# Optimization experiments

Hardware: AMD Instinct MI355X
Metric: run time of the kernel (lower is better)

Reference implementation:

```python
import jax, jax.numpy as jnp
import numpy as np
from bisect import bisect

# hyperparameters (from init_kwargs)
DELTA = 1e-4
GAMMA = 0.1
UTILITY_SCALE = -0.01
PRIORITY_RAIL = 0.5
LOSS_BALANCE = 1.0
ALPHA_ELU = 1.0
ENTROPY_THRESHOLDS = [0, 10, 50]
ENTROPY_LEVELS = [0.0, 0.05, 0.1, 1.0]
MASK_LEVEL = 10000.0

N = 512


def setup_inputs() -> dict:
    key = jax.random.key(0)
    k1, k2, k3, k4 = jax.random.split(key, 4)
    soft_adj = jax.random.uniform(k1, (N, N), dtype=jnp.float32)
    # original adjacency is a binary {0,1} float mask
    original_adj = (jax.random.uniform(k2, (N, N)) > 0.5).astype(jnp.float32)
    distances = jax.random.uniform(k3, (N, N), dtype=jnp.float32) * 100.0
    flow = jax.random.uniform(k4, (N, N), dtype=jnp.float32) * 10.0
    epoch = 20  # python int, selects entropy penalty level via bisect
    return {"soft_adj": soft_adj, "original_adj": original_adj,
            "distances": distances, "flow": flow, "epoch": epoch}


def _shortest_path(soft_adj, distances):
    """Soft (softmin via logsumexp) Floyd-Warshall all-pairs shortest path."""
    W = distances / (soft_adj + DELTA)          # [N, N] effective edge weights
    n = W.shape[0]
    w0 = W * (1.0 - jnp.eye(n, dtype=W.dtype))  # zero diagonal

    def step(w, k):
        # softmin(w, w[:,k,None] + w[None,k,:]) without materializing a stack
        path_through_k = w[:, k][:, None] + w[k, :][None, :]
        w_new = -GAMMA * jnp.logaddexp(-w / GAMMA, -path_through_k / GAMMA)
        return w_new, None

    w_dist, _ = jax.lax.scan(step, w0, jnp.arange(n))
    return w_dist


def reference(soft_adj, original_adj, distances, flow, epoch):
    loss_cost = jnp.sum(soft_adj * distances)

    shortest_paths = _shortest_path(soft_adj, distances)

    exp_ut_rail = jnp.exp(UTILITY_SCALE * shortest_paths * PRIORITY_RAIL)
    exp_ut_base = jnp.exp(UTILITY_SCALE * distances)
    choice_matrix = exp_ut_rail / (exp_ut_rail + exp_ut_base)
    distance_saved = distances - PRIORITY_RAIL * shortest_paths
    utility_gain = flow * choice_matrix * distance_saved
    utility_gain = jax.nn.elu(utility_gain, alpha=ALPHA_ELU) + ALPHA_ELU

    inverse_soft = jnp.eye(soft_adj.shape[0], dtype=soft_adj.dtype) - soft_adj
    entropy_loss = jnp.sum(jnp.square(soft_adj * inverse_soft))
    entropy_scale = ENTROPY_LEVELS[bisect(ENTROPY_THRESHOLDS, epoch)]

    mask_loss = jnp.sum(soft_adj * (1.0 - original_adj))

    return (loss_cost
            + LOSS_BALANCE * jnp.sum(utility_gain)
            + entropy_loss * entropy_scale
            + MASK_LEVEL * mask_loss)
```

## Files before the change

kernel.cpp:

```cpp
#include <hip/hip_runtime.h>
#include <math.h>

#define NN 512
#define KP 64
#define NPANEL 8
#define NTHR 256
#define NBLK 256
#define TRUNITS (448 * 112)

#define D_   0
#define V_   4160
#define B2_  8320
#define UB_  12672
#define SB_  17024
#define H_   21376
#define LDSN 25728

__device__ __forceinline__ float einit(const float* s, const float* dI, int i, int j) {
  float w = dI[i * NN + j] / (s[i * NN + j] + 1e-4f);
  if (i == j) w = 0.f;
  return expf(-10.f * w);
}

__global__ __launch_bounds__(NTHR) void fw_p0(
    const float* __restrict__ s, const float* __restrict__ dI,
    float* __restrict__ Cs, float* __restrict__ Rs, float* __restrict__ out) {
  __shared__ __align__(16) float lds[LDSN];
  const int blk = blockIdx.x, tid = threadIdx.x;
  const bool isC = (blk < 16);
  const int sb = (blk >> 1) & 7;
  const int h = blk & 1;
  const int sOff = sb * KP;
  const bool haveSl = (sb != 0);
  if (blk == 0 && tid == 0) out[0] = 0.f;

  for (int e = tid; e < 4096; e += NTHR) {
    const int a = e >> 6, b = e & 63;
    lds[D_ + a * 65 + b] = einit(s, dI, a, b);
  }
  if (haveSl) {
    if (isC) {
      for (int e = tid; e < 2048; e += NTHR) {
        const int a = 32 * h + (e >> 6), b = e & 63;
        lds[V_ + a * 65 + b] = einit(s, dI, sOff + a, b);
      }
    } else {
      for (int e = tid; e < 2048; e += NTHR) {
        const int m = e >> 5, j = 32 * h + (e & 31);
        lds[V_ + j * 65 + m] = einit(s, dI, m, sOff + j);
      }
    }
  }
  __syncthreads();

  if (tid < 64) {
    float x[64];
    if (isC) {
#pragma unroll
      for (int a = 0; a < 64; ++a) x[a] = lds[D_ + a * 65 + tid];
    } else {
#pragma unroll
      for (int a = 0; a < 64; ++a) x[a] = lds[D_ + tid * 65 + a];
    }
#pragma unroll
    for (int m = 0; m < 64; ++m) {
      const float xm = x[m];
      lds[H_ + m * 68 + tid] = xm;
#pragma unroll
      for (int a = 0; a < 64; ++a) {
        const int sa = __builtin_amdgcn_readlane(__float_as_int(x[a]), m);
        x[a] += __int_as_float(sa) * xm;
      }
    }
  } else if (tid < 192) {
    if (!haveSl) {
      for (int e = tid - 64; e < 4096; e += 128) {
        const int a = e >> 6, b = e & 63;
        lds[V_ + a * 65 + b] = isC ? lds[D_ + a * 65 + b] : lds[D_ + b * 65 + a];
      }
    }
  }
  __syncthreads();

  for (int cch = 0; cch < 4; ++cch) {
    const int mb = cch * 16;
    if (cch > 0 && tid < 128) {
      const int r = 32 * h + (tid & 31);
      const int g = tid >> 5;
      const int m0c = mb + 4 * g;
      const int vb = V_ + r * 65;
      float a0 = lds[vb + m0c + 0], a1 = lds[vb + m0c + 1];
      float a2 = lds[vb + m0c + 2], a3 = lds[vb + m0c + 3];
      for (int mp = 0; mp < mb; ++mp) {
        const float vr = lds[vb + mp];
        const float4 u4 = *(const float4*)&lds[H_ + mp * 68 + m0c];
        a0 += vr * u4.x; a1 += vr * u4.y; a2 += vr * u4.z; a3 += vr * u4.w;
      }
      lds[vb + m0c + 0] = a0; lds[vb + m0c + 1] = a1;
      lds[vb + m0c + 2] = a2; lds[vb + m0c + 3] = a3;
    }
    __syncthreads();
    if (tid < 32) {
      const int r = 32 * h + tid;
      const int vb = V_ + r * 65 + mb;
      float v[16];
#pragma unroll
      for (int u2 = 0; u2 < 16; ++u2) v[u2] = lds[vb + u2];
#pragma unroll
      for (int mp = 0; mp < 15; ++mp) {
        const float vmp = v[mp];
#pragma unroll
        for (int m2 = mp + 1; m2 < 16; ++m2)
          v[m2] += vmp * lds[H_ + (mb + mp) * 68 + (mb + m2)];
      }
#pragma unroll
      for (int u2 = 0; u2 < 16; ++u2) lds[vb + u2] = v[u2];
    }
    __syncthreads();
  }

  if (isC) {
    for (int e = tid; e < 2048; e += NTHR) {
      const int a = 32 * h + (e >> 6), b = e & 63;
      Cs[(size_t)(sOff + a) * KP + b] = lds[V_ + a * 65 + b];
    }
  } else {
    for (int e = tid; e < 2048; e += NTHR) {
      const int m = e >> 5, j = 32 * h + (e & 31);
      Rs[(size_t)m * NN + (sOff + j)] = lds[V_ + j * 65 + m];
    }
  }
}

__global__ __launch_bounds__(NTHR) void fw_phase(
    const float* __restrict__ s, const float* __restrict__ dI,
    float* __restrict__ E, float* __restrict__ Cs, float* __restrict__ Rs,
    int p) {
  __shared__ __align__(16) float lds[LDSN];
  const int blk = blockIdx.x, tid = threadIdx.x;
  const int k0 = p * KP;
  const float* Cprev = Cs + (size_t)(p - 1) * (NN * KP);
  const float* Rprev = Rs + (size_t)(p - 1) * (KP * NN);

  if (blk >= 32) {
    const int gt = (blk - 32) * NTHR + tid;
    if (gt >= TRUNITS) return;
    const int ii = gt / 112;
    const int jj = gt - ii * 112;
    const int i = (ii < k0) ? ii : ii + KP;
    const int j = ((jj < (p << 4)) ? jj : jj + 16) << 2;
    const int idx = i * NN + j;
    float4 acc;
    if (p == 1) {
      acc.x = einit(s, dI, i, j + 0);
      acc.y = einit(s, dI, i, j + 1);
      acc.z = einit(s, dI, i, j + 2);
      acc.w = einit(s, dI, i, j + 3);
    } else {
      acc = *(const float4*)(E + idx);
    }
    const float* crow = Cprev + (size_t)i * KP;
    const float* rcol = Rprev + j;
#pragma unroll 8
    for (int r = 0; r < KP; ++r) {
      const float cv = crow[r];
      const float4 rv = *(const float4*)(rcol + (size_t)r * NN);
      acc.x += cv * rv.x; acc.y += cv * rv.y;
      acc.z += cv * rv.z; acc.w += cv * rv.w;
    }
    *(float4*)(E + idx) = acc;
    return;
  }

  const bool isC = (blk < 16);
  const int sb = (blk >> 1) & 7;
  const int h = blk & 1;
  const int sOff = sb * KP;
  const bool haveSl = (sb != p);

  const int r0d = (tid >> 4) << 2, m0d = (tid & 15) << 2;
  float4 epre[4];
  if (p == 1) {
#pragma unroll
    for (int i2 = 0; i2 < 4; ++i2) {
      epre[i2].x = einit(s, dI, k0 + r0d + i2, k0 + m0d + 0);
      epre[i2].y = einit(s, dI, k0 + r0d + i2, k0 + m0d + 1);
      epre[i2].z = einit(s, dI, k0 + r0d + i2, k0 + m0d + 2);
      epre[i2].w = einit(s, dI, k0 + r0d + i2, k0 + m0d + 3);
    }
  } else {
#pragma unroll
    for (int i2 = 0; i2 < 4; ++i2)
      epre[i2] = *(const float4*)(E + (size_t)(k0 + r0d + i2) * NN + (k0 + m0d));
  }

#pragma unroll
  for (int k = 0; k < 4; ++k) {
    const int e4 = tid + k * NTHR;
    const int a = e4 >> 4, b4 = (e4 & 15) << 2;
    *(float4*)&lds[B2_ + a * 68 + b4] =
        *(const float4*)(Cprev + (size_t)(k0 + a) * KP + b4);
    *(float4*)&lds[UB_ + a * 68 + b4] =
        *(const float4*)(Rprev + (size_t)a * NN + (k0 + b4));
    if (haveSl) {
      if (isC)
        *(float4*)&lds[SB_ + a * 68 + b4] =
            *(const float4*)(Cprev + (size_t)(sOff + a) * KP + b4);
      else
        *(float4*)&lds[SB_ + a * 68 + b4] =
            *(const float4*)(Rprev + (size_t)a * NN + (sOff + b4));
    }
  }
  __syncthreads();

  {
    float acc[4][4];
#pragma unroll
    for (int i2 = 0; i2 < 4; ++i2) {
      acc[i2][0] = epre[i2].x; acc[i2][1] = epre[i2].y;
      acc[i2][2] = epre[i2].z; acc[i2][3] = epre[i2].w;
    }
    for (int rr = 0; rr < KP; ++rr) {
      const float4 b4 = *(const float4*)&lds[UB_ + rr * 68 + m0d];
#pragma unroll
      for (int i2 = 0; i2 < 4; ++i2) {
        const float av = lds[B2_ + (r0d + i2) * 68 + rr];
        acc[i2][0] += av * b4.x; acc[i2][1] += av * b4.y;
        acc[i2][2] += av * b4.z; acc[i2][3] += av * b4.w;
      }
    }
#pragma unroll
    for (int i2 = 0; i2 < 4; ++i2)
#pragma unroll
      for (int j2 = 0; j2 < 4; ++j2)
        lds[D_ + (r0d + i2) * 65 + (m0d + j2)] = acc[i2][j2];
  }
  __syncthreads();

  if (tid < 64) {
    float x[64];
    if (isC) {
#pragma unroll
      for (int a = 0; a < 64; ++a) x[a] = lds[D_ + a * 65 + tid];
    } else {
#pragma unroll
      for (int a = 0; a < 64; ++a) x[a] = lds[D_ + tid * 65 + a];
    }
#pragma unroll
    for (int m = 0; m < 64; ++m) {
      const float xm = x[m];
      lds[H_ + m * 68 + tid] = xm;
#pragma unroll
      for (int a = 0; a < 64; ++a) {
        const int sa = __builtin_amdgcn_readlane(__float_as_int(x[a]), m);
        x[a] += __int_as_float(sa) * xm;
      }
    }
  } else if (tid < 192) {
    const int tt = tid - 64;
    if (haveSl) {
      float acc[4][4];
      if (isC) {
        const int r0 = 32 * h + ((tt >> 4) << 2);
        const int m0 = (tt & 15) << 2;
        if (p == 1) {
#pragma unroll
          for (int i2 = 0; i2 < 4; ++i2) {
            acc[i2][0] = einit(s, dI, sOff + r0 + i2, k0 + m0 + 0);
            acc[i2][1] = einit(s, dI, sOff + r0 + i2, k0 + m0 + 1);
            acc[i2][2] = einit(s, dI, sOff + r0 + i2, k0 + m0 + 2);
            acc[i2][3] = einit(s, dI, sOff + r0 + i2, k0 + m0 + 3);
          }
        } else {
#pragma unroll
          for (int i2 = 0; i2 < 4; ++i2) {
            const float4 ev = *(const float4*)(E + (size_t)(sOff + r0 + i2) * NN + (k0 + m0));
            acc[i2][0] = ev.x; acc[i2][1] = ev.y; acc[i2][2] = ev.z; acc[i2][3] = ev.w;
          }
        }
        for (int rr = 0; rr < KP; ++rr) {
          const float4 b4 = *(const float4*)&lds[UB_ + rr * 68 + m0];
#pragma unroll
          for (int i2 = 0; i2 < 4; ++i2) {
            const float av = lds[SB_ + (r0 + i2) * 68 + rr];
            acc[i2][0] += av * b4.x; acc[i2][1] += av * b4.y;
            acc[i2][2] += av * b4.z; acc[i2][3] += av * b4.w;
          }
        }
#pragma unroll
        for (int i2 = 0; i2 < 4; ++i2) {
          *(float4*)(E + (size_t)(sOff + r0 + i2) * NN + (k0 + m0)) =
              make_float4(acc[i2][0], acc[i2][1], acc[i2][2], acc[i2][3]);
#pragma unroll
          for (int j2 = 0; j2 < 4; ++j2)
            lds[V_ + (r0 + i2) * 65 + (m0 + j2)] = acc[i2][j2];
        }
      } else {
        const int r0 = (tt & 15) << 2;
        const int c0 = 32 * h + ((tt >> 4) << 2);
        if (p == 1) {
#pragma unroll
          for (int i2 = 0; i2 < 4; ++i2) {
            acc[i2][0] = einit(s, dI, k0 + r0 + i2, sOff + c0 + 0);
            acc[i2][1] = einit(s, dI, k0 + r0 + i2, sOff + c0 + 1);
            acc[i2][2] = einit(s, dI, k0 + r0 + i2, sOff + c0 + 2);
            acc[i2][3] = einit(s, dI, k0 + r0 + i2, sOff + c0 + 3);
          }
        } else {
#pragma unroll
          for (int i2 = 0; i2 < 4; ++i2) {
            const float4 ev = *(const float4*)(E + (size_t)(k0 + r0 + i2) * NN + (sOff + c0));
            acc[i2][0] = ev.x; acc[i2][1] = ev.y; acc[i2][2] = ev.z; acc[i2][3] = ev.w;
          }
        }
        for (int rr = 0; rr < KP; ++rr) {
          const float4 b4 = *(const float4*)&lds[SB_ + rr * 68 + c0];
#pragma unroll
          for (int i2 = 0; i2 < 4; ++i2) {
            const float av = lds[B2_ + (r0 + i2) * 68 + rr];
            acc[i2][0] += av * b4.x; acc[i2][1] += av * b4.y;
            acc[i2][2] += av * b4.z; acc[i2][3] += av * b4.w;
          }
        }
#pragma unroll
        for (int i2 = 0; i2 < 4; ++i2) {
          *(float4*)(E + (size_t)(k0 + r0 + i2) * NN + (sOff + c0)) =
              make_float4(acc[i2][0], acc[i2][1], acc[i2][2], acc[i2][3]);
#pragma unroll
          for (int j2 = 0; j2 < 4; ++j2)
            lds[V_ + (c0 + j2) * 65 + (r0 + i2)] = acc[i2][j2];
        }
      }
    } else {
      for (int e = tt; e < 4096; e += 128) {
        const int a = e >> 6, b = e & 63;
        lds[V_ + a * 65 + b] = isC ? lds[D_ + a * 65 + b] : lds[D_ + b * 65 + a];
      }
    }
  } else {
    if (p == 1 && !haveSl && isC) {
      for (int e = 2048 * h + (tid - 192); e < 2048 * (h + 1); e += 64) {
        const int a = e >> 6, b = e & 63;
        E[(size_t)(k0 + a) * NN + (k0 + b)] = einit(s, dI, k0 + a, k0 + b);
      }
    }
  }
  __syncthreads();

  for (int cch = 0; cch < 4; ++cch) {
    const int mb = cch * 16;
    if (cch > 0 && tid < 128) {
      const int r = 32 * h + (tid & 31);
      const int g = tid >> 5;
      const int m0c = mb + 4 * g;
      const int vb = V_ + r * 65;
      float a0 = lds[vb + m0c + 0], a1 = lds[vb + m0c + 1];
      float a2 = lds[vb + m0c + 2], a3 = lds[vb + m0c + 3];
      for (int mp = 0; mp < mb; ++mp) {
        const float vr = lds[vb + mp];
        const float4 u4 = *(const float4*)&lds[H_ + mp * 68 + m0c];
        a0 += vr * u4.x; a1 += vr * u4.y; a2 += vr * u4.z; a3 += vr * u4.w;
      }
      lds[vb + m0c + 0] = a0; lds[vb + m0c + 1] = a1;
      lds[vb + m0c + 2] = a2; lds[vb + m0c + 3] = a3;
    }
    __syncthreads();
    if (tid < 32) {
      const int r = 32 * h + tid;
      const int vb = V_ + r * 65 + mb;
      float v[16];
#pragma unroll
      for (int u2 = 0; u2 < 16; ++u2) v[u2] = lds[vb + u2];
#pragma unroll
      for (int mp = 0; mp < 15; ++mp) {
        const float vmp = v[mp];
#pragma unroll
        for (int m2 = mp + 1; m2 < 16; ++m2)
          v[m2] += vmp * lds[H_ + (mb + mp) * 68 + (mb + m2)];
      }
#pragma unroll
      for (int u2 = 0; u2 < 16; ++u2) lds[vb + u2] = v[u2];
    }
    __syncthreads();
  }

  float* Cp = Cs + (size_t)p * (NN * KP);
  float* Rp = Rs + (size_t)p * (KP * NN);
  if (isC) {
    for (int e = tid; e < 2048; e += NTHR) {
      const int a = 32 * h + (e >> 6), b = e & 63;
      Cp[(size_t)(sOff + a) * KP + b] = lds[V_ + a * 65 + b];
    }
  } else {
    for (int e = tid; e < 2048; e += NTHR) {
      const int m = e >> 5, j = 32 * h + (e & 31);
      Rp[(size_t)m * NN + (sOff + j)] = lds[V_ + j * 65 + m];
    }
  }
}

__device__ __forceinline__ float loss_elem(float Ev, float sv, float ov,
                                           float dv, float fv, int i, int j,
                                           float esc) {
  const float sp = (Ev > 0.f) ? (-0.1f * logf(Ev)) : 1e9f;
  const float ur = expf(-0.005f * sp);
  const float ub = expf(-0.01f * dv);
  const float choice = ur / (ur + ub);
  const float ug = fv * choice * (dv - 0.5f * sp);
  const float util = (ug > 0.f) ? (ug + 1.f) : expf(ug);
  const float ent = sv * (((i == j) ? 1.f : 0.f) - sv);
  return sv * dv + util + esc * ent * ent + 10000.f * (sv * (1.f - ov));
}

__global__ __launch_bounds__(NTHR) void k_loss(
    const float* __restrict__ s, const float* __restrict__ o,
    const float* __restrict__ dI, const float* __restrict__ f,
    const int* __restrict__ ep, const float* __restrict__ E,
    const float* __restrict__ Cs, const float* __restrict__ Rs,
    float* __restrict__ out) {
  __shared__ float red[NTHR];
  const int tid = threadIdx.x;
  const int g = blockIdx.x * NTHR + tid;
  const int idx0 = g * 4;
  const int i = idx0 >> 9;
  const int j = idx0 & (NN - 1);
  const float* C7 = Cs + (size_t)7 * (NN * KP);
  const float* R7 = Rs + (size_t)7 * (KP * NN);
  float4 acc = *(const float4*)(E + idx0);
  {
    const float* crow = C7 + (size_t)i * KP;
    const float* rcol = R7 + j;
#pragma unroll 8
    for (int r = 0; r < KP; ++r) {
      const float cv = crow[r];
      const float4 rv = *(const float4*)(rcol + (size_t)r * NN);
      acc.x += cv * rv.x; acc.y += cv * rv.y;
      acc.z += cv * rv.z; acc.w += cv * rv.w;
    }
  }
  const int bi = i >> 6, bj = j >> 6;
  if (bi == bj && bi >= 1) {
    const float* cf = Cs + (size_t)(bi - 1) * (NN * KP) + (size_t)i * KP;
    const float* rf = Rs + (size_t)(bi - 1) * (KP * NN) + j;
#pragma unroll 8
    for (int r = 0; r < KP; ++r) {
      const float cv = cf[r];
      const float4 rv = *(const float4*)(rf + (size_t)r * NN);
      acc.x += cv * rv.x; acc.y += cv * rv.y;
      acc.z += cv * rv.z; acc.w += cv * rv.w;
    }
  }
  const float4 sv = *(const float4*)(s + idx0);
  const float4 ov = *(const float4*)(o + idx0);
  const float4 dv = *(const float4*)(dI + idx0);
  const float4 fv = *(const float4*)(f + idx0);
  const int e = ep[0];
  const float esc = (e < 0) ? 0.f : (e < 10) ? 0.05f : (e < 50) ? 0.1f : 1.f;
  float lsum = loss_elem(acc.x, sv.x, ov.x, dv.x, fv.x, i, j + 0, esc)
             + loss_elem(acc.y, sv.y, ov.y, dv.y, fv.y, i, j + 1, esc)
             + loss_elem(acc.z, sv.z, ov.z, dv.z, fv.z, i, j + 2, esc)
             + loss_elem(acc.w, sv.w, ov.w, dv.w, fv.w, i, j + 3, esc);
  red[tid] = lsum;
  __syncthreads();
#pragma unroll
  for (int st = 128; st > 0; st >>= 1) {
    if (tid < st) red[tid] += red[tid + st];
    __syncthreads();
  }
  if (tid == 0) atomicAdd(out, red[0]);
}

extern "C" void kernel_launch(void* const* d_in, const int* in_sizes, int n_in,
                              void* d_out, int out_size, void* d_ws, size_t ws_size,
                              hipStream_t stream) {
  const float* s = (const float*)d_in[0];
  const float* o = (const float*)d_in[1];
  const float* d = (const float*)d_in[2];
  const float* f = (const float*)d_in[3];
  const int* ep = (const int*)d_in[4];

  float* E = (float*)d_ws;
  float* Cs = E + NN * NN;
  float* Rs = Cs + NPANEL * NN * KP;
  float* out = (float*)d_out;

  fw_p0<<<32, NTHR, 0, stream>>>(s, d, Cs, Rs, out);
  for (int p = 1; p < NPANEL; ++p)
    fw_phase<<<NBLK, NTHR, 0, stream>>>(s, d, E, Cs, Rs, p);
  k_loss<<<NBLK, NTHR, 0, stream>>>(s, o, d, f, ep, E, Cs, Rs, out);
}
```

Baseline: 246.8 us.

## Fuse all Floyd-Warshall phases and loss into one persistent kernel with grid barriers

Replaces the nine separate kernel launches (panel 0, seven phase kernels, loss) with a single persistent kernel of 256 blocks that synchronises phases through a hierarchical atomic grid barrier in workspace flags. The flags are cleared with a memset before launch. This aims to remove per-launch overhead and the idle gaps between dependent kernels. It assumes all 256 blocks are co-resident; otherwise the barrier deadlocks. It also adds atomic spin-wait cost at each phase boundary.

Measured after the change: 397.7 us. 1.61x slower.

```diff
diff --git a/kernel.cpp b/kernel.cpp
--- a/kernel.cpp
+++ b/kernel.cpp
@@ -22,381 +22,25 @@
   return expf(-10.f * w);
 }
 
-__global__ __launch_bounds__(NTHR) void fw_p0(
-    const float* __restrict__ s, const float* __restrict__ dI,
-    float* __restrict__ Cs, float* __restrict__ Rs, float* __restrict__ out) {
-  __shared__ __align__(16) float lds[LDSN];
-  const int blk = blockIdx.x, tid = threadIdx.x;
-  const bool isC = (blk < 16);
-  const int sb = (blk >> 1) & 7;
-  const int h = blk & 1;
-  const int sOff = sb * KP;
-  const bool haveSl = (sb != 0);
-  if (blk == 0 && tid == 0) out[0] = 0.f;
-
-  for (int e = tid; e < 4096; e += NTHR) {
-    const int a = e >> 6, b = e & 63;
-    lds[D_ + a * 65 + b] = einit(s, dI, a, b);
-  }
-  if (haveSl) {
-    if (isC) {
-      for (int e = tid; e < 2048; e += NTHR) {
-        const int a = 32 * h + (e >> 6), b = e & 63;
-        lds[V_ + a * 65 + b] = einit(s, dI, sOff + a, b);
-      }
-    } else {
-      for (int e = tid; e < 2048; e += NTHR) {
-        const int m = e >> 5, j = 32 * h + (e & 31);
-        lds[V_ + j * 65 + m] = einit(s, dI, m, sOff + j);
-      }
-    }
+__device__ __forceinline__ void gridbar(unsigned* flags, int ph, int blk, int tid) {
+  __syncthreads();
+  if (tid == 0) {
+    __threadfence();
+    unsigned v = __hip_atomic_fetch_add(&flags[blk & 7], 1u, __ATOMIC_RELEASE,
+                                        __HIP_MEMORY_SCOPE_AGENT);
+    if (v == 32u * (unsigned)(ph + 1) - 1u) {
+      unsigned r = __hip_atomic_fetch_add(&flags[8], 1u, __ATOMIC_RELEASE,
+                                          __HIP_MEMORY_SCOPE_AGENT);
+      if (r == 8u * (unsigned)(ph + 1) - 1u)
+        __hip_atomic_store(&flags[9], (unsigned)(ph + 1), __ATOMIC_RELEASE,
+                           __HIP_MEMORY_SCOPE_AGENT);
+    }
+    while (__hip_atomic_load(&flags[9], __ATOMIC_RELAXED,
+                             __HIP_MEMORY_SCOPE_AGENT) < (unsigned)(ph + 1))
+      __builtin_amdgcn_s_sleep(4);
+    __builtin_amdgcn_fence(__ATOMIC_ACQUIRE, "agent");
   }
   __syncthreads();
-
-  if (tid < 64) {
-    float x[64];
-    if (isC) {
-#pragma unroll
-      for (int a = 0; a < 64; ++a) x[a] = lds[D_ + a * 65 + tid];
-    } else {
-#pragma unroll
-      for (int a = 0; a < 64; ++a) x[a] = lds[D_ + tid * 65 + a];
-    }
-#pragma unroll
-    for (int m = 0; m < 64; ++m) {
-      const float xm = x[m];
-      lds[H_ + m * 68 + tid] = xm;
-#pragma unroll
-      for (int a = 0; a < 64; ++a) {
-        const int sa = __builtin_amdgcn_readlane(__float_as_int(x[a]), m);
-        x[a] += __int_as_float(sa) * xm;
-      }
-    }
-  } else if (tid < 192) {
-    if (!haveSl) {
-      for (int e = tid - 64; e < 4096; e += 128) {
-        const int a = e >> 6, b = e & 63;
-        lds[V_ + a * 65 + b] = isC ? lds[D_ + a * 65 + b] : lds[D_ + b * 65 + a];
-      }
-    }
-  }
-  __syncthreads();
-
-  for (int cch = 0; cch < 4; ++cch) {
-    const int mb = cch * 16;
-    if (cch > 0 && tid < 128) {
-      const int r = 32 * h + (tid & 31);
-      const int g = tid >> 5;
-      const int m0c = mb + 4 * g;
-      const int vb = V_ + r * 65;
-      float a0 = lds[vb + m0c + 0], a1 = lds[vb + m0c + 1];
-      float a2 = lds[vb + m0c + 2], a3 = lds[vb + m0c + 3];
-      for (int mp = 0; mp < mb; ++mp) {
-        const float vr = lds[vb + mp];
-        const float4 u4 = *(const float4*)&lds[H_ + mp * 68 + m0c];
-        a0 += vr * u4.x; a1 += vr * u4.y; a2 += vr * u4.z; a3 += vr * u4.w;
-      }
-      lds[vb + m0c + 0] = a0; lds[vb + m0c + 1] = a1;
-      lds[vb + m0c + 2] = a2; lds[vb + m0c + 3] = a3;
-    }
-    __syncthreads();
-    if (tid < 32) {
-      const int r = 32 * h + tid;
-      const int vb = V_ + r * 65 + mb;
-      float v[16];
-#pragma unroll
-      for (int u2 = 0; u2 < 16; ++u2) v[u2] = lds[vb + u2];
-#pragma unroll
-      for (int mp = 0; mp < 15; ++mp) {
-        const float vmp = v[mp];
-#pragma unroll
-        for (int m2 = mp + 1; m2 < 16; ++m2)
-          v[m2] += vmp * lds[H_ + (mb + mp) * 68 + (mb + m2)];
-      }
-#pragma unroll
-      for (int u2 = 0; u2 < 16; ++u2) lds[vb + u2] = v[u2];
-    }
-    __syncthreads();
-  }
-
-  if (isC) {
-    for (int e = tid; e < 2048; e += NTHR) {
-      const int a = 32 * h + (e >> 6), b = e & 63;
-      Cs[(size_t)(sOff + a) * KP + b] = lds[V_ + a * 65 + b];
-    }
-  } else {
-    for (int e = tid; e < 2048; e += NTHR) {
-      const int m = e >> 5, j = 32 * h + (e & 31);
-      Rs[(size_t)m * NN + (sOff + j)] = lds[V_ + j * 65 + m];
-    }
-  }
-}
-
-__global__ __launch_bounds__(NTHR) void fw_phase(
-    const float* __restrict__ s, const float* __restrict__ dI,
-    float* __restrict__ E, float* __restrict__ Cs, float* __restrict__ Rs,
-    int p) {
-  __shared__ __align__(16) float lds[LDSN];
-  const int blk = blockIdx.x, tid = threadIdx.x;
-  const int k0 = p * KP;
-  const float* Cprev = Cs + (size_t)(p - 1) * (NN * KP);
-  const float* Rprev = Rs + (size_t)(p - 1) * (KP * NN);
-
-  if (blk >= 32) {
-    const int gt = (blk - 32) * NTHR + tid;
-    if (gt >= TRUNITS) return;
-    const int ii = gt / 112;
-    const int jj = gt - ii * 112;
-    const int i = (ii < k0) ? ii : ii + KP;
-    const int j = ((jj < (p << 4)) ? jj : jj + 16) << 2;
-    const int idx = i * NN + j;
-    float4 acc;
-    if (p == 1) {
-      acc.x = einit(s, dI, i, j + 0);
-      acc.y = einit(s, dI, i, j + 1);
-      acc.z = einit(s, dI, i, j + 2);
-      acc.w = einit(s, dI, i, j + 3);
-    } else {
-      acc = *(const float4*)(E + idx);
-    }
-    const float* crow = Cprev + (size_t)i * KP;
-    const float* rcol = Rprev + j;
-#pragma unroll 8
-    for (int r = 0; r < KP; ++r) {
-      const float cv = crow[r];
-      const float4 rv = *(const float4*)(rcol + (size_t)r * NN);
-      acc.x += cv * rv.x; acc.y += cv * rv.y;
-      acc.z += cv * rv.z; acc.w += cv * rv.w;
-    }
-    *(float4*)(E + idx) = acc;
-    return;
-  }
-
-  const bool isC = (blk < 16);
-  const int sb = (blk >> 1) & 7;
-  const int h = blk & 1;
-  const int sOff = sb * KP;
-  const bool haveSl = (sb != p);
-
-  const int r0d = (tid >> 4) << 2, m0d = (tid & 15) << 2;
-  float4 epre[4];
-  if (p == 1) {
-#pragma unroll
-    for (int i2 = 0; i2 < 4; ++i2) {
-      epre[i2].x = einit(s, dI, k0 + r0d + i2, k0 + m0d + 0);
-      epre[i2].y = einit(s, dI, k0 + r0d + i2, k0 + m0d + 1);
-      epre[i2].z = einit(s, dI, k0 + r0d + i2, k0 + m0d + 2);
-      epre[i2].w = einit(s, dI, k0 + r0d + i2, k0 + m0d + 3);
-    }
-  } else {
-#pragma unroll
-    for (int i2 = 0; i2 < 4; ++i2)
-      epre[i2] = *(const float4*)(E + (size_t)(k0 + r0d + i2) * NN + (k0 + m0d));
-  }
-
-#pragma unroll
-  for (int k = 0; k < 4; ++k) {
-    const int e4 = tid + k * NTHR;
-    const int a = e4 >> 4, b4 = (e4 & 15) << 2;
-    *(float4*)&lds[B2_ + a * 68 + b4] =
-        *(const float4*)(Cprev + (size_t)(k0 + a) * KP + b4);
-    *(float4*)&lds[UB_ + a * 68 + b4] =
-        *(const float4*)(Rprev + (size_t)a * NN + (k0 + b4));
-    if (haveSl) {
-      if (isC)
-        *(float4*)&lds[SB_ + a * 68 + b4] =
-            *(const float4*)(Cprev + (size_t)(sOff + a) * KP + b4);
-      else
-        *(float4*)&lds[SB_ + a * 68 + b4] =
-            *(const float4*)(Rprev + (size_t)a * NN + (sOff + b4));
-    }
-  }
-  __syncthreads();
-
-  {
-    float acc[4][4];
-#pragma unroll
-    for (int i2 = 0; i2 < 4; ++i2) {
-      acc[i2][0] = epre[i2].x; acc[i2][1] = epre[i2].y;
-      acc[i2][2] = epre[i2].z; acc[i2][3] = epre[i2].w;
-    }
-    for (int rr = 0; rr < KP; ++rr) {
-      const float4 b4 = *(const float4*)&lds[UB_ + rr * 68 + m0d];
-#pragma unroll
-      for (int i2 = 0; i2 < 4; ++i2) {
-        const float av = lds[B2_ + (r0d + i2) * 68 + rr];
-        acc[i2][0] += av * b4.x; acc[i2][1] += av * b4.y;
-        acc[i2][2] += av * b4.z; acc[i2][3] += av * b4.w;
-      }
-    }
-#pragma unroll
-    for (int i2 = 0; i2 < 4; ++i2)
-#pragma unroll
-      for (int j2 = 0; j2 < 4; ++j2)
-        lds[D_ + (r0d + i2) * 65 + (m0d + j2)] = acc[i2][j2];
-  }
-  __syncthreads();
-
-  if (tid < 64) {
-    float x[64];
-    if (isC) {
-#pragma unroll
-      for (int a = 0; a < 64; ++a) x[a] = lds[D_ + a * 65 + tid];
-    } else {
-#pragma unroll
-      for (int a = 0; a < 64; ++a) x[a] = lds[D_ + tid * 65 + a];
-    }
-#pragma unroll
-    for (int m = 0; m < 64; ++m) {
-      const float xm = x[m];
-      lds[H_ + m * 68 + tid] = xm;
-#pragma unroll
-      for (int a = 0; a < 64; ++a) {
-        const int sa = __builtin_amdgcn_readlane(__float_as_int(x[a]), m);
-        x[a] += __int_as_float(sa) * xm;
-      }
-    }
-  } else if (tid < 192) {
-    const int tt = tid - 64;
-    if (haveSl) {
-      float acc[4][4];
-      if (isC) {
-        const int r0 = 32 * h + ((tt >> 4) << 2);
-        const int m0 = (tt & 15) << 2;
-        if (p == 1) {
-#pragma unroll
-          for (int i2 = 0; i2 < 4; ++i2) {
-            acc[i2][0] = einit(s, dI, sOff + r0 + i2, k0 + m0 + 0);
-            acc[i2][1] = einit(s, dI, sOff + r0 + i2, k0 + m0 + 1);
-            acc[i2][2] = einit(s, dI, sOff + r0 + i2, k0 + m0 + 2);
-            acc[i2][3] = einit(s, dI, sOff + r0 + i2, k0 + m0 + 3);
-          }
-        } else {
-#pragma unroll
-          for (int i2 = 0; i2 < 4; ++i2) {
-            const float4 ev = *(const float4*)(E + (size_t)(sOff + r0 + i2) * NN + (k0 + m0));
-            acc[i2][0] = ev.x; acc[i2][1] = ev.y; acc[i2][2] = ev.z; acc[i2][3] = ev.w;
-          }
-        }
-        for (int rr = 0; rr < KP; ++rr) {
-          const float4 b4 = *(const float4*)&lds[UB_ + rr * 68 + m0];
-#pragma unroll
-          for (int i2 = 0; i2 < 4; ++i2) {
-            const float av = lds[SB_ + (r0 + i2) * 68 + rr];
-            acc[i2][0] += av * b4.x; acc[i2][1] += av * b4.y;
-            acc[i2][2] += av * b4.z; acc[i2][3] += av * b4.w;
-          }
-        }
-#pragma unroll
-        for (int i2 = 0; i2 < 4; ++i2) {
-          *(float4*)(E + (size_t)(sOff + r0 + i2) * NN + (k0 + m0)) =
-              make_float4(acc[i2][0], acc[i2][1], acc[i2][2], acc[i2][3]);
-#pragma unroll
-          for (int j2 = 0; j2 < 4; ++j2)
-            lds[V_ + (r0 + i2) * 65 + (m0 + j2)] = acc[i2][j2];
-        }
-      } else {
-        const int r0 = (tt & 15) << 2;
-        const int c0 = 32 * h + ((tt >> 4) << 2);
-        if (p == 1) {
-#pragma unroll
-          for (int i2 = 0; i2 < 4; ++i2) {
-            acc[i2][0] = einit(s, dI, k0 + r0 + i2, sOff + c0 + 0);
-            acc[i2][1] = einit(s, dI, k0 + r0 + i2, sOff + c0 + 1);
-            acc[i2][2] = einit(s, dI, k0 + r0 + i2, sOff + c0 + 2);
-            acc[i2][3] = einit(s, dI, k0 + r0 + i2, sOff + c0 + 3);
-          }
-        } else {
-#pragma unroll
-          for (int i2 = 0; i2 < 4; ++i2) {
-            const float4 ev = *(const float4*)(E + (size_t)(k0 + r0 + i2) * NN + (sOff + c0));
-            acc[i2][0] = ev.x; acc[i2][1] = ev.y; acc[i2][2] = ev.z; acc[i2][3] = ev.w;
-          }
-        }
-        for (int rr = 0; rr < KP; ++rr) {
-          const float4 b4 = *(const float4*)&lds[SB_ + rr * 68 + c0];
-#pragma unroll
-          for (int i2 = 0; i2 < 4; ++i2) {
-            const float av = lds[B2_ + (r0 + i2) * 68 + rr];
-            acc[i2][0] += av * b4.x; acc[i2][1] += av * b4.y;
-            acc[i2][2] += av * b4.z; acc[i2][3] += av * b4.w;
-          }
-        }
-#pragma unroll
-        for (int i2 = 0; i2 < 4; ++i2) {
-          *(float4*)(E + (size_t)(k0 + r0 + i2) * NN + (sOff + c0)) =
-              make_float4(acc[i2][0], acc[i2][1], acc[i2][2], acc[i2][3]);
-#pragma unroll
-          for (int j2 = 0; j2 < 4; ++j2)
-            lds[V_ + (c0 + j2) * 65 + (r0 + i2)] = acc[i2][j2];
-        }
-      }
-    } else {
-      for (int e = tt; e < 4096; e += 128) {
-        const int a = e >> 6, b = e & 63;
-        lds[V_ + a * 65 + b] = isC ? lds[D_ + a * 65 + b] : lds[D_ + b * 65 + a];
-      }
-    }
-  } else {
-    if (p == 1 && !haveSl && isC) {
-      for (int e = 2048 * h + (tid - 192); e < 2048 * (h + 1); e += 64) {
-        const int a = e >> 6, b = e & 63;
-        E[(size_t)(k0 + a) * NN + (k0 + b)] = einit(s, dI, k0 + a, k0 + b);
-      }
-    }
-  }
-  __syncthreads();
-
-  for (int cch = 0; cch < 4; ++cch) {
-    const int mb = cch * 16;
-    if (cch > 0 && tid < 128) {
-      const int r = 32 * h + (tid & 31);
-      const int g = tid >> 5;
-      const int m0c = mb + 4 * g;
-      const int vb = V_ + r * 65;
-      float a0 = lds[vb + m0c + 0], a1 = lds[vb + m0c + 1];
-      float a2 = lds[vb + m0c + 2], a3 = lds[vb + m0c + 3];
-      for (int mp = 0; mp < mb; ++mp) {
-        const float vr = lds[vb + mp];
-        const float4 u4 = *(const float4*)&lds[H_ + mp * 68 + m0c];
-        a0 += vr * u4.x; a1 += vr * u4.y; a2 += vr * u4.z; a3 += vr * u4.w;
-      }
-      lds[vb + m0c + 0] = a0; lds[vb + m0c + 1] = a1;
-      lds[vb + m0c + 2] = a2; lds[vb + m0c + 3] = a3;
-    }
-    __syncthreads();
-    if (tid < 32) {
-      const int r = 32 * h + tid;
-      const int vb = V_ + r * 65 + mb;
-      float v[16];
-#pragma unroll
-      for (int u2 = 0; u2 < 16; ++u2) v[u2] = lds[vb + u2];
-#pragma unroll
-      for (int mp = 0; mp < 15; ++mp) {
-        const float vmp = v[mp];
-#pragma unroll
-        for (int m2 = mp + 1; m2 < 16; ++m2)
-          v[m2] += vmp * lds[H_ + (mb + mp) * 68 + (mb + m2)];
-      }
-#pragma unroll
-      for (int u2 = 0; u2 < 16; ++u2) lds[vb + u2] = v[u2];
-    }
-    __syncthreads();
-  }
-
-  float* Cp = Cs + (size_t)p * (NN * KP);
-  float* Rp = Rs + (size_t)p * (KP * NN);
-  if (isC) {
-    for (int e = tid; e < 2048; e += NTHR) {
-      const int a = 32 * h + (e >> 6), b = e & 63;
-      Cp[(size_t)(sOff + a) * KP + b] = lds[V_ + a * 65 + b];
-    }
-  } else {
-    for (int e = tid; e < 2048; e += NTHR) {
-      const int m = e >> 5, j = 32 * h + (e & 31);
-      Rp[(size_t)m * NN + (sOff + j)] = lds[V_ + j * 65 + m];
-    }
-  }
 }
 
 __device__ __forceinline__ float loss_elem(float Ev, float sv, float ov,
@@ -412,62 +56,430 @@
   return sv * dv + util + esc * ent * ent + 10000.f * (sv * (1.f - ov));
 }
 
-__global__ __launch_bounds__(NTHR) void k_loss(
+__global__ __launch_bounds__(NTHR) void fw_all(
     const float* __restrict__ s, const float* __restrict__ o,
     const float* __restrict__ dI, const float* __restrict__ f,
-    const int* __restrict__ ep, const float* __restrict__ E,
-    const float* __restrict__ Cs, const float* __restrict__ Rs,
-    float* __restrict__ out) {
-  __shared__ float red[NTHR];
-  const int tid = threadIdx.x;
-  const int g = blockIdx.x * NTHR + tid;
-  const int idx0 = g * 4;
-  const int i = idx0 >> 9;
-  const int j = idx0 & (NN - 1);
-  const float* C7 = Cs + (size_t)7 * (NN * KP);
-  const float* R7 = Rs + (size_t)7 * (KP * NN);
-  float4 acc = *(const float4*)(E + idx0);
+    const int* __restrict__ ep, float* __restrict__ E,
+    float* __restrict__ Cs, float* __restrict__ Rs,
+    unsigned* __restrict__ flags, float* __restrict__ out) {
+  __shared__ __align__(16) float lds[LDSN];
+  const int blk = blockIdx.x, tid = threadIdx.x;
+  const bool panel = (blk < 32);
+  const bool isC = (blk < 16);
+  const int sb = (blk >> 1) & 7;
+  const int h = blk & 1;
+  const int sOff = sb * KP;
+
+  if (panel) {
+    const bool haveSl = (sb != 0);
+    for (int e = tid; e < 4096; e += NTHR) {
+      const int a = e >> 6, b = e & 63;
+      lds[D_ + a * 65 + b] = einit(s, dI, a, b);
+    }
+    if (haveSl) {
+      if (isC) {
+        for (int e = tid; e < 2048; e += NTHR) {
+          const int a = 32 * h + (e >> 6), b = e & 63;
+          lds[V_ + a * 65 + b] = einit(s, dI, sOff + a, b);
+        }
+      } else {
+        for (int e = tid; e < 2048; e += NTHR) {
+          const int m = e >> 5, j = 32 * h + (e & 31);
+          lds[V_ + j * 65 + m] = einit(s, dI, m, sOff + j);
+        }
+      }
+    }
+    __syncthreads();
+    if (tid < 64) {
+      float x[64];
+      if (isC) {
+#pragma unroll
+        for (int a = 0; a < 64; ++a) x[a] = lds[D_ + a * 65 + tid];
+      } else {
+#pragma unroll
+        for (int a = 0; a < 64; ++a) x[a] = lds[D_ + tid * 65 + a];
+      }
+#pragma unroll
+      for (int m = 0; m < 64; ++m) {
+        const float xm = x[m];
+        lds[H_ + m * 68 + tid] = xm;
+#pragma unroll
+        for (int a = 0; a < 64; ++a) {
+          const int sa = __builtin_amdgcn_readlane(__float_as_int(x[a]), m);
+          x[a] += __int_as_float(sa) * xm;
+        }
+      }
+    } else if (tid < 192) {
+      if (!haveSl) {
+        for (int e = tid - 64; e < 4096; e += 128) {
+          const int a = e >> 6, b = e & 63;
+          lds[V_ + a * 65 + b] = isC ? lds[D_ + a * 65 + b] : lds[D_ + b * 65 + a];
+        }
+      }
+    }
+    __syncthreads();
+    for (int cch = 0; cch < 4; ++cch) {
+      const int mb = cch * 16;
+      if (cch > 0 && tid < 128) {
+        const int r = 32 * h + (tid & 31);
+        const int g = tid >> 5;
+        const int m0c = mb + 4 * g;
+        const int vb = V_ + r * 65;
+        float a0 = lds[vb + m0c + 0], a1 = lds[vb + m0c + 1];
+        float a2 = lds[vb + m0c + 2], a3 = lds[vb + m0c + 3];
+        for (int mp = 0; mp < mb; ++mp) {
+          const float vr = lds[vb + mp];
+          const float4 u4 = *(const float4*)&lds[H_ + mp * 68 + m0c];
+          a0 += vr * u4.x; a1 += vr * u4.y; a2 += vr * u4.z; a3 += vr * u4.w;
+        }
+        lds[vb + m0c + 0] = a0; lds[vb + m0c + 1] = a1;
+        lds[vb + m0c + 2] = a2; lds[vb + m0c + 3] = a3;
+      }
+      __syncthreads();
+      if (tid < 32) {
+        const int r = 32 * h + tid;
+        const int vb = V_ + r * 65 + mb;
+        float v[16];
+#pragma unroll
+        for (int u2 = 0; u2 < 16; ++u2) v[u2] = lds[vb + u2];
+#pragma unroll
+        for (int mp = 0; mp < 15; ++mp) {
+          const float vmp = v[mp];
+#pragma unroll
+          for (int m2 = mp + 1; m2 < 16; ++m2)
+            v[m2] += vmp * lds[H_ + (mb + mp) * 68 + (mb + m2)];
+        }
+#pragma unroll
+        for (int u2 = 0; u2 < 16; ++u2) lds[vb + u2] = v[u2];
+      }
+      __syncthreads();
+    }
+    if (isC) {
+      for (int e = tid; e < 2048; e += NTHR) {
+        const int a = 32 * h + (e >> 6), b = e & 63;
+        Cs[(size_t)(sOff + a) * KP + b] = lds[V_ + a * 65 + b];
+      }
+    } else {
+      for (int e = tid; e < 2048; e += NTHR) {
+        const int m = e >> 5, j = 32 * h + (e & 31);
+        Rs[(size_t)m * NN + (sOff + j)] = lds[V_ + j * 65 + m];
+      }
+    }
+  } else if (blk == 32 && tid == 0) {
+    out[0] = 0.f;
+  }
+  gridbar(flags, 0, blk, tid);
+
+  for (int p = 1; p < NPANEL; ++p) {
+    const int k0 = p * KP;
+    const float* Cprev = Cs + (size_t)(p - 1) * (NN * KP);
+    const float* Rprev = Rs + (size_t)(p - 1) * (KP * NN);
+
+    if (!panel) {
+      const int gt = (blk - 32) * NTHR + tid;
+      if (gt < TRUNITS) {
+        const int ii = gt / 112;
+        const int jj = gt - ii * 112;
+        const int i = (ii < k0) ? ii : ii + KP;
+        const int j = ((jj < (p << 4)) ? jj : jj + 16) << 2;
+        const int idx = i * NN + j;
+        float4 acc;
+        if (p == 1) {
+          acc.x = einit(s, dI, i, j + 0);
+          acc.y = einit(s, dI, i, j + 1);
+          acc.z = einit(s, dI, i, j + 2);
+          acc.w = einit(s, dI, i, j + 3);
+        } else {
+          acc = *(const float4*)(E + idx);
+        }
+        const float* crow = Cprev + (size_t)i * KP;
+        const float* rcol = Rprev + j;
+#pragma unroll 8
+        for (int r = 0; r < KP; ++r) {
+          const float cv = crow[r];
+          const float4 rv = *(const float4*)(rcol + (size_t)r * NN);
+          acc.x += cv * rv.x; acc.y += cv * rv.y;
+          acc.z += cv * rv.z; acc.w += cv * rv.w;
+        }
+        *(float4*)(E + idx) = acc;
+      }
+    } else {
+      const bool haveSl = (sb != p);
+      const int r0d = (tid >> 4) << 2, m0d = (tid & 15) << 2;
+      float4 epre[4];
+      if (p == 1) {
+#pragma unroll
+        for (int i2 = 0; i2 < 4; ++i2) {
+          epre[i2].x = einit(s, dI, k0 + r0d + i2, k0 + m0d + 0);
+          epre[i2].y = einit(s, dI, k0 + r0d + i2, k0 + m0d + 1);
+          epre[i2].z = einit(s, dI, k0 + r0d + i2, k0 + m0d + 2);
+          epre[i2].w = einit(s, dI, k0 + r0d + i2, k0 + m0d + 3);
+        }
+      } else {
+#pragma unroll
+        for (int i2 = 0; i2 < 4; ++i2)
+          epre[i2] = *(const float4*)(E + (size_t)(k0 + r0d + i2) * NN + (k0 + m0d));
+      }
+
+#pragma unroll
+      for (int k = 0; k < 4; ++k) {
+        const int e4 = tid + k * NTHR;
+        const int a = e4 >> 4, b4 = (e4 & 15) << 2;
+        *(float4*)&lds[B2_ + a * 68 + b4] =
+            *(const float4*)(Cprev + (size_t)(k0 + a) * KP + b4);
+        *(float4*)&lds[UB_ + a * 68 + b4] =
+            *(const float4*)(Rprev + (size_t)a * NN + (k0 + b4));
+        if (haveSl) {
+          if (isC)
+            *(float4*)&lds[SB_ + a * 68 + b4] =
+                *(const float4*)(Cprev + (size_t)(sOff + a) * KP + b4);
+          else
+            *(float4*)&lds[SB_ + a * 68 + b4] =
+                *(const float4*)(Rprev + (size_t)a * NN + (sOff + b4));
+        }
+      }
+      __syncthreads();
+
+      {
+        float acc[4][4];
+#pragma unroll
+        for (int i2 = 0; i2 < 4; ++i2) {
+          acc[i2][0] = epre[i2].x; acc[i2][1] = epre[i2].y;
+          acc[i2][2] = epre[i2].z; acc[i2][3] = epre[i2].w;
+        }
+        for (int rr = 0; rr < KP; ++rr) {
+          const float4 b4 = *(const float4*)&lds[UB_ + rr * 68 + m0d];
+#pragma unroll
+          for (int i2 = 0; i2 < 4; ++i2) {
+            const float av = lds[B2_ + (r0d + i2) * 68 + rr];
+            acc[i2][0] += av * b4.x; acc[i2][1] += av * b4.y;
+            acc[i2][2] += av * b4.z; acc[i2][3] += av * b4.w;
+          }
+        }
+#pragma unroll
+        for (int i2 = 0; i2 < 4; ++i2)
+#pragma unroll
+          for (int j2 = 0; j2 < 4; ++j2)
+            lds[D_ + (r0d + i2) * 65 + (m0d + j2)] = acc[i2][j2];
+      }
+      __syncthreads();
+
+      if (tid < 64) {
+        float x[64];
+        if (isC) {
+#pragma unroll
+          for (int a = 0; a < 64; ++a) x[a] = lds[D_ + a * 65 + tid];
+        } else {
+#pragma unroll
+          for (int a = 0; a < 64; ++a) x[a] = lds[D_ + tid * 65 + a];
+        }
+#pragma unroll
+        for (int m = 0; m < 64; ++m) {
+          const float xm = x[m];
+          lds[H_ + m * 68 + tid] = xm;
+#pragma unroll
+          for (int a = 0; a < 64; ++a) {
+            const int sa = __builtin_amdgcn_readlane(__float_as_int(x[a]), m);
+            x[a] += __int_as_float(sa) * xm;
+          }
+        }
+      } else if (tid < 192) {
+        const int tt = tid - 64;
+        if (haveSl) {
+          float acc[4][4];
+          if (isC) {
+            const int r0 = 32 * h + ((tt >> 4) << 2);
+            const int m0 = (tt & 15) << 2;
+            if (p == 1) {
+#pragma unroll
+              for (int i2 = 0; i2 < 4; ++i2) {
+                acc[i2][0] = einit(s, dI, sOff + r0 + i2, k0 + m0 + 0);
+                acc[i2][1] = einit(s, dI, sOff + r0 + i2, k0 + m0 + 1);
+                acc[i2][2] = einit(s, dI, sOff + r0 + i2, k0 + m0 + 2);
+                acc[i2][3] = einit(s, dI, sOff + r0 + i2, k0 + m0 + 3);
+              }
+            } else {
+#pragma unroll
+              for (int i2 = 0; i2 < 4; ++i2) {
+                const float4 ev = *(const float4*)(E + (size_t)(sOff + r0 + i2) * NN + (k0 + m0));
+                acc[i2][0] = ev.x; acc[i2][1] = ev.y; acc[i2][2] = ev.z; acc[i2][3] = ev.w;
+              }
+            }
+            for (int rr = 0; rr < KP; ++rr) {
+              const float4 b4 = *(const float4*)&lds[UB_ + rr * 68 + m0];
+#pragma unroll
+              for (int i2 = 0; i2 < 4; ++i2) {
+                const float av = lds[SB_ + (r0 + i2) * 68 + rr];
+                acc[i2][0] += av * b4.x; acc[i2][1] += av * b4.y;
+                acc[i2][2] += av * b4.z; acc[i2][3] += av * b4.w;
+              }
+            }
+#pragma unroll
+            for (int i2 = 0; i2 < 4; ++i2) {
+              *(float4*)(E + (size_t)(sOff + r0 + i2) * NN + (k0 + m0)) =
+                  make_float4(acc[i2][0], acc[i2][1], acc[i2][2], acc[i2][3]);
+#pragma unroll
+              for (int j2 = 0; j2 < 4; ++j2)
+                lds[V_ + (r0 + i2) * 65 + (m0 + j2)] = acc[i2][j2];
+            }
+          } else {
+            const int r0 = (tt & 15) << 2;
+            const int c0 = 32 * h + ((tt >> 4) << 2);
+            if (p == 1) {
+#pragma unroll
+              for (int i2 = 0; i2 < 4; ++i2) {
+                acc[i2][0] = einit(s, dI, k0 + r0 + i2, sOff + c0 + 0);
+                acc[i2][1] = einit(s, dI, k0 + r0 + i2, sOff + c0 + 1);
+                acc[i2][2] = einit(s, dI, k0 + r0 + i2, sOff + c0 + 2);
+                acc[i2][3] = einit(s, dI, k0 + r0 + i2, sOff + c0 + 3);
+              }
+            } else {
+#pragma unroll
+              for (int i2 = 0; i2 < 4; ++i2) {
+                const float4 ev = *(const float4*)(E + (size_t)(k0 + r0 + i2) * NN + (sOff + c0));
+                acc[i2][0] = ev.x; acc[i2][1] = ev.y; acc[i2][2] = ev.z; acc[i2][3] = ev.w;
+              }
+            }
+            for (int rr = 0; rr < KP; ++rr) {
+              const float4 b4 = *(const float4*)&lds[SB_ + rr * 68 + c0];
+#pragma unroll
+              for (int i2 = 0; i2 < 4; ++i2) {
+                const float av = lds[B2_ + (r0 + i2) * 68 + rr];
+                acc[i2][0] += av * b4.x; acc[i2][1] += av * b4.y;
+                acc[i2][2] += av * b4.z; acc[i2][3] += av * b4.w;
+              }
+            }
+#pragma unroll
+            for (int i2 = 0; i2 < 4; ++i2) {
+              *(float4*)(E + (size_t)(k0 + r0 + i2) * NN + (sOff + c0)) =
+                  make_float4(acc[i2][0], acc[i2][1], acc[i2][2], acc[i2][3]);
+#pragma unroll
+              for (int j2 = 0; j2 < 4; ++j2)
+                lds[V_ + (c0 + j2) * 65 + (r0 + i2)] = acc[i2][j2];
+            }
+          }
+        } else {
+          for (int e = tt; e < 4096; e += 128) {
+            const int a = e >> 6, b = e & 63;
+            lds[V_ + a * 65 + b] = isC ? lds[D_ + a * 65 + b] : lds[D_ + b * 65 + a];
+          }
+        }
+      } else {
+        if (p == 1 && !haveSl && isC) {
+          for (int e = 2048 * h + (tid - 192); e < 2048 * (h + 1); e += 64) {
+            const int a = e >> 6, b = e & 63;
+            E[(size_t)(k0 + a) * NN + (k0 + b)] = einit(s, dI, k0 + a, k0 + b);
+          }
+        }
+      }
+      __syncthreads();
+
+      for (int cch = 0; cch < 4; ++cch) {
+        const int mb = cch * 16;
+        if (cch > 0 && tid < 128) {
+          const int r = 32 * h + (tid & 31);
+          const int g = tid >> 5;
+          const int m0c = mb + 4 * g;
+          const int vb = V_ + r * 65;
+          float a0 = lds[vb + m0c + 0], a1 = lds[vb + m0c + 1];
+          float a2 = lds[vb + m0c + 2], a3 = lds[vb + m0c + 3];
+          for (int mp = 0; mp < mb; ++mp) {
+            const float vr = lds[vb + mp];
+            const float4 u4 = *(const float4*)&lds[H_ + mp * 68 + m0c];
+            a0 += vr * u4.x; a1 += vr * u4.y; a2 += vr * u4.z; a3 += vr * u4.w;
+          }
+          lds[vb + m0c + 0] = a0; lds[vb + m0c + 1] = a1;
+          lds[vb + m0c + 2] = a2; lds[vb + m0c + 3] = a3;
+        }
+        __syncthreads();
+        if (tid < 32) {
+          const int r = 32 * h + tid;
+          const int vb = V_ + r * 65 + mb;
+          float v[16];
+#pragma unroll
+          for (int u2 = 0; u2 < 16; ++u2) v[u2] = lds[vb + u2];
+#pragma unroll
+          for (int mp = 0; mp < 15; ++mp) {
+            const float vmp = v[mp];
+#pragma unroll
+            for (int m2 = mp + 1; m2 < 16; ++m2)
+              v[m2] += vmp * lds[H_ + (mb + mp) * 68 + (mb + m2)];
+          }
+#pragma unroll
+          for (int u2 = 0; u2 < 16; ++u2) lds[vb + u2] = v[u2];
+        }
+        __syncthreads();
+      }
+
+      float* Cp = Cs + (size_t)p * (NN * KP);
+      float* Rp = Rs + (size_t)p * (KP * NN);
+      if (isC) {
+        for (int e = tid; e < 2048; e += NTHR) {
+          const int a = 32 * h + (e >> 6), b = e & 63;
+          Cp[(size_t)(sOff + a) * KP + b] = lds[V_ + a * 65 + b];
+        }
+      } else {
+        for (int e = tid; e < 2048; e += NTHR) {
+          const int m = e >> 5, j = 32 * h + (e & 31);
+          Rp[(size_t)m * NN + (sOff + j)] = lds[V_ + j * 65 + m];
+        }
+      }
+    }
+    gridbar(flags, p, blk, tid);
+  }
+
   {
-    const float* crow = C7 + (size_t)i * KP;
-    const float* rcol = R7 + j;
+    const int g = blk * NTHR + tid;
+    const int idx0 = g * 4;
+    const int i = idx0 >> 9;
+    const int j = idx0 & (NN - 1);
+    const float* C7 = Cs + (size_t)7 * (NN * KP);
+    const float* R7 = Rs + (size_t)7 * (KP * NN);
+    float4 acc = *(const float4*)(E + idx0);
+    {
+      const float* crow = C7 + (size_t)i * KP;
+      const float* rcol = R7 + j;
 #pragma unroll 8
-    for (int r = 0; r < KP; ++r) {
-      const float cv = crow[r];
-      const float4 rv = *(const float4*)(rcol + (size_t)r * NN);
-      acc.x += cv * rv.x; acc.y += cv * rv.y;
-      acc.z += cv * rv.z; acc.w += cv * rv.w;
-    }
+      for (int r = 0; r < KP; ++r) {
+        const float cv = crow[r];
+        const float4 rv = *(const float4*)(rcol + (size_t)r * NN);
+        acc.x += cv * rv.x; acc.y += cv * rv.y;
+        acc.z += cv * rv.z; acc.w += cv * rv.w;
+      }
+    }
+    const int bi = i >> 6, bj = j >> 6;
+    if (bi == bj && bi >= 1) {
+      const float* cf = Cs + (size_t)(bi - 1) * (NN * KP) + (size_t)i * KP;
+      const float* rf = Rs + (size_t)(bi - 1) * (KP * NN) + j;
+#pragma unroll 8
+      for (int r = 0; r < KP; ++r) {
+        const float cv = cf[r];
+        const float4 rv = *(const float4*)(rf + (size_t)r * NN);
+        acc.x += cv * rv.x; acc.y += cv * rv.y;
+        acc.z += cv * rv.z; acc.w += cv * rv.w;
+      }
+    }
+    const float4 sv = *(const float4*)(s + idx0);
+    const float4 ov = *(const float4*)(o + idx0);
+    const float4 dv = *(const float4*)(dI + idx0);
+    const float4 fv = *(const float4*)(f + idx0);
+    const int e = ep[0];
+    const float esc = (e < 0) ? 0.f : (e < 10) ? 0.05f : (e < 50) ? 0.1f : 1.f;
+    float lsum = loss_elem(acc.x, sv.x, ov.x, dv.x, fv.x, i, j + 0, esc)
+               + loss_elem(acc.y, sv.y, ov.y, dv.y, fv.y, i, j + 1, esc)
+               + loss_elem(acc.z, sv.z, ov.z, dv.z, fv.z, i, j + 2, esc)
+               + loss_elem(acc.w, sv.w, ov.w, dv.w, fv.w, i, j + 3, esc);
+    float* red = lds;
+    __syncthreads();
+    red[tid] = lsum;
+    __syncthreads();
+#pragma unroll
+    for (int st = 128; st > 0; st >>= 1) {
+      if (tid < st) red[tid] += red[tid + st];
+      __syncthreads();
+    }
+    if (tid == 0) atomicAdd(out, red[0]);
   }
-  const int bi = i >> 6, bj = j >> 6;
-  if (bi == bj && bi >= 1) {
-    const float* cf = Cs + (size_t)(bi - 1) * (NN * KP) + (size_t)i * KP;
-    const float* rf = Rs + (size_t)(bi - 1) * (KP * NN) + j;
-#pragma unroll 8
-    for (int r = 0; r < KP; ++r) {
-      const float cv = cf[r];
-      const float4 rv = *(const float4*)(rf + (size_t)r * NN);
-      acc.x += cv * rv.x; acc.y += cv * rv.y;
-      acc.z += cv * rv.z; acc.w += cv * rv.w;
-    }
-  }
-  const float4 sv = *(const float4*)(s + idx0);
-  const float4 ov = *(const float4*)(o + idx0);
-  const float4 dv = *(const float4*)(dI + idx0);
-  const float4 fv = *(const float4*)(f + idx0);
-  const int e = ep[0];
-  const float esc = (e < 0) ? 0.f : (e < 10) ? 0.05f : (e < 50) ? 0.1f : 1.f;
-  float lsum = loss_elem(acc.x, sv.x, ov.x, dv.x, fv.x, i, j + 0, esc)
-             + loss_elem(acc.y, sv.y, ov.y, dv.y, fv.y, i, j + 1, esc)
-             + loss_elem(acc.z, sv.z, ov.z, dv.z, fv.z, i, j + 2, esc)
-             + loss_elem(acc.w, sv.w, ov.w, dv.w, fv.w, i, j + 3, esc);
-  red[tid] = lsum;
-  __syncthreads();
-#pragma unroll
-  for (int st = 128; st > 0; st >>= 1) {
-    if (tid < st) red[tid] += red[tid + st];
-    __syncthreads();
-  }
-  if (tid == 0) atomicAdd(out, red[0]);
 }
 
 extern "C" void kernel_launch(void* const* d_in, const int* in_sizes, int n_in,
@@ -479,13 +491,12 @@
   const float* f = (const float*)d_in[3];
   const int* ep = (const int*)d_in[4];
 
-  float* E = (float*)d_ws;
+  unsigned* flags = (unsigned*)d_ws;
+  float* E = (float*)((char*)d_ws + 256);
   float* Cs = E + NN * NN;
   float* Rs = Cs + NPANEL * NN * KP;
   float* out = (float*)d_out;
 
-  fw_p0<<<32, NTHR, 0, stream>>>(s, d, Cs, Rs, out);
-  for (int p = 1; p < NPANEL; ++p)
-    fw_phase<<<NBLK, NTHR, 0, stream>>>(s, d, E, Cs, Rs, p);
-  k_loss<<<NBLK, NTHR, 0, stream>>>(s, o, d, f, ep, E, Cs, Rs, out);
+  hipMemsetAsync(d_ws, 0, 256, stream);
+  fw_all<<<NBLK, NTHR, 0, stream>>>(s, o, d, f, ep, E, Cs, Rs, flags, out);
 }
```
